# Performance work log

Hardware: AMD Instinct MI355X
Metric: run time of the kernel (lower is better)

The kernel has to match this reference:

```python
import jax, jax.numpy as jnp
import numpy as np

N, E = 20000, 320000
NF, EF = 4, 4
HID, HEADS, MODEL_HID = 128, 4, 128


def _p(key, shape, scale=0.1):
    return scale * jax.random.normal(key, shape, dtype=jnp.float32)


def setup_inputs() -> dict:
    key = jax.random.key(0)
    ks = jax.random.split(key, 32)
    x = jax.random.normal(ks[0], (N, NF), dtype=jnp.float32)
    src = jax.random.randint(ks[1], (E,), 0, N)
    off = jax.random.randint(ks[2], (E,), 1, N)
    dst = (src + off) % N  # no self-loops (PyG removes then re-adds them)
    edge_index = jnp.stack([src, dst]).astype(jnp.int64)
    edge_attr = jax.random.uniform(ks[3], (E, EF), dtype=jnp.float32)
    d = dict(x=x, edge_index=edge_index, edge_attr=edge_attr)
    # input_proj
    d['Wp'] = _p(ks[4], (NF, HID)); d['bp'] = jnp.zeros((HID,), jnp.float32)
    # GAT layer 1: in=HID, heads=HEADS, out=HID, concat
    d['W1'] = _p(ks[5], (HID, HEADS * HID)); d['We1'] = _p(ks[6], (EF, HEADS * HID))
    d['as1'] = _p(ks[7], (HEADS, HID)); d['ad1'] = _p(ks[8], (HEADS, HID)); d['ae1'] = _p(ks[9], (HEADS, HID))
    d['b1'] = jnp.zeros((HEADS * HID,), jnp.float32)
    d['g1'] = jnp.ones((HEADS * HID,), jnp.float32); d['be1'] = jnp.zeros((HEADS * HID,), jnp.float32)
    # GAT layer 2: in=HEADS*HID, heads=1, out=HID, mean
    d['W2'] = _p(ks[10], (HEADS * HID, HID)); d['We2'] = _p(ks[11], (EF, HID))
    d['as2'] = _p(ks[12], (1, HID)); d['ad2'] = _p(ks[13], (1, HID)); d['ae2'] = _p(ks[14], (1, HID))
    d['b2'] = jnp.zeros((HID,), jnp.float32)
    d['g2'] = jnp.ones((HID,), jnp.float32); d['be2'] = jnp.zeros((HID,), jnp.float32)
    # output proj + importance scorer
    d['Wo'] = _p(ks[15], (HID, MODEL_HID)); d['bo'] = jnp.zeros((MODEL_HID,), jnp.float32)
    d['Wi'] = _p(ks[16], (MODEL_HID, 1)); d['bi'] = jnp.zeros((1,), jnp.float32)
    return d


def _layer_norm(x, g, b, eps=1e-5):
    mu = x.mean(-1, keepdims=True)
    v = ((x - mu) ** 2).mean(-1, keepdims=True)
    return (x - mu) * jax.lax.rsqrt(v + eps) * g + b


def _segment_softmax(logits, seg, num):
    m = jax.ops.segment_max(logits, seg, num_segments=num)
    e = jnp.exp(logits - m[seg])
    d = jax.ops.segment_sum(e, seg, num_segments=num)
    return e / d[seg]


def _forward(x, edge_index, edge_attr, Wp, bp, W1, We1, as1, ad1, ae1, b1, g1, be1,
             W2, We2, as2, ad2, ae2, b2, g2, be2, Wo, bo, Wi, bi):
    n = x.shape[0]
    src, dst = edge_index[0], edge_index[1]
    e = edge_attr.shape[0]
    # add_self_loops with fill_value='mean': self-loop attr = mean of incoming edge_attr
    deg = jax.ops.segment_sum(jnp.ones((e,), edge_attr.dtype), dst, num_segments=n)
    loop_attr = jax.ops.segment_sum(edge_attr, dst, num_segments=n) / jnp.maximum(deg, 1.0)[:, None]
    loops = jnp.arange(n)
    src_f = jnp.concatenate([src, loops])
    dst_f = jnp.concatenate([dst, loops])
    ea = jnp.concatenate([edge_attr, loop_attr], axis=0)  # [E+N, EF]

    def gat(h, W, We, a_s, a_d, a_e, bias, heads, out_c, concat):
        xh = (h @ W).reshape(n, heads, out_c)                 # [N,H,C]
        eh = (ea @ We).reshape(-1, heads, out_c)              # [E+N,H,C]
        al_s = (xh * a_s).sum(-1)                             # [N,H]
        al_d = (xh * a_d).sum(-1)                             # [N,H]
        al_e = (eh * a_e).sum(-1)                             # [E+N,H]
        logits = jax.nn.leaky_relu(al_s[src_f] + al_d[dst_f] + al_e, negative_slope=0.2)
        alpha = _segment_softmax(logits, dst_f, n)            # [E+N,H]
        out = jax.ops.segment_sum(xh[src_f] * alpha[..., None], dst_f, num_segments=n)
        out = out.reshape(n, heads * out_c) if concat else out.mean(axis=1)
        return out + bias, alpha

    h = x @ Wp + bp
    h, _ = gat(h, W1, We1, as1, ad1, ae1, b1, HEADS, HID, True)
    h = jax.nn.elu(_layer_norm(h, g1, be1))  # dropout is a no-op in eval
    h, edge_attention = gat(h, W2, We2, as2, ad2, ae2, b2, 1, HID, False)
    h = _layer_norm(h, g2, be2)
    emb = h @ Wo + bo
    importance = jax.nn.sigmoid(emb @ Wi + bi).squeeze(-1)
    return emb, edge_attention, importance


def reference(x, edge_index, edge_attr, Wp, bp, W1, We1, as1, ad1, ae1, b1, g1, be1,
              W2, We2, as2, ad2, ae2, b2, g2, be2, Wo, bo, Wi, bi):
    return _forward(x, edge_index, edge_attr, Wp, bp, W1, We1, as1, ad1, ae1, b1, g1, be1,
                    W2, We2, as2, ad2, ae2, b2, g2, be2, Wo, bo, Wi, bi)
```

## Files before the change

kernel.cpp:

```cpp
#include <hip/hip_runtime.h>
#include <math.h>
#include <stdint.h>

#define N_NODES 20000
#define N_EDGES 320000
#define EN_TOT  340000
#define CAP     160

typedef __attribute__((ext_vector_type(8))) _Float16 half8v;
typedef __attribute__((ext_vector_type(2))) _Float16 half2v;
typedef __attribute__((ext_vector_type(4))) float float4v;

__device__ __forceinline__ ushort f2h(float f) {
    _Float16 h = (_Float16)f;
    return __builtin_bit_cast(ushort, h);
}
__device__ __forceinline__ float h2f(ushort s) {
    return (float)__builtin_bit_cast(_Float16, s);
}

__global__ void k_deg(const int* __restrict__ dst, int* __restrict__ degi) {
    int e = blockIdx.x * 256 + threadIdx.x;
    if (e >= N_EDGES) return;
    atomicAdd(&degi[dst[e]], 1);
}

__global__ __launch_bounds__(1024) void k_scan(const int* __restrict__ degi, int* __restrict__ offsets,
                                               const float* __restrict__ We1, const float* __restrict__ ae1,
                                               const float* __restrict__ We2, const float* __restrict__ ae2,
                                               float* __restrict__ M1, float* __restrict__ m2) {
    __shared__ int s[1024];
    int t = threadIdx.x;
    int n0 = t * 20;
    int tot = 0;
    for (int i = 0; i < 20; i++) {
        int n = n0 + i;
        if (n < N_NODES) tot += degi[n] + 1;
    }
    s[t] = tot;
    __syncthreads();
    for (int off = 1; off < 1024; off <<= 1) {
        int v = (t >= off) ? s[t - off] : 0;
        __syncthreads();
        s[t] += v;
        __syncthreads();
    }
    int run = s[t] - tot;
    for (int i = 0; i < 20; i++) {
        int n = n0 + i;
        if (n < N_NODES) {
            offsets[n] = run;
            run += degi[n] + 1;
        }
    }
    if (t == 1023) offsets[N_NODES] = s[1023];
    if (t < 16) {
        int f = t >> 2, h = t & 3;
        float acc = 0.f;
        for (int c = 0; c < 128; c++) acc += We1[f * 512 + h * 128 + c] * ae1[h * 128 + c];
        M1[f * 4 + h] = acc;
    } else if (t < 20) {
        int f = t - 16;
        float acc = 0.f;
        for (int c = 0; c < 128; c++) acc += We2[f * 128 + c] * ae2[c];
        m2[f] = acc;
    }
}

__global__ void k_fill(const int* __restrict__ src, const int* __restrict__ dst,
                       const int* __restrict__ offsets, int* __restrict__ cursor,
                       int2* __restrict__ csr_se) {
    int i = blockIdx.x * 256 + threadIdx.x;
    if (i >= EN_TOT) return;
    int d, sidx, eid;
    if (i < N_EDGES) { d = dst[i]; sidx = src[i]; eid = i; }
    else { int n = i - N_EDGES; d = n; sidx = n; eid = N_EDGES + n; }
    int pos = offsets[d] + atomicAdd(&cursor[d], 1);
    csr_se[pos] = make_int2(sidx, eid);
}

__global__ __launch_bounds__(256) void k_misc(const int* __restrict__ offsets, const int2* __restrict__ csr_se,
                                              const float* __restrict__ eattr, float* __restrict__ loopattr,
                                              const float* __restrict__ W1, const float* __restrict__ W2,
                                              const float* __restrict__ Wo, ushort* __restrict__ W1T,
                                              ushort* __restrict__ W2T, ushort* __restrict__ WoT,
                                              const float* __restrict__ x, const float* __restrict__ Wp,
                                              const float* __restrict__ bp, ushort* __restrict__ h0h) {
    int b = blockIdx.x;
    int tid = threadIdx.x;
    if (b < 5000) {
        int wv = tid >> 6, l = tid & 63;
        int n = b * 4 + wv;
        if (n >= N_NODES) return;
        int start = offsets[n], end = offsets[n + 1];
        float sx = 0.f, sy = 0.f, sz = 0.f, sw = 0.f;
        for (int p = start + l; p < end; p += 64) {
            int eid = csr_se[p].y;
            if (eid < N_EDGES) {
                float4 e = *(const float4*)&eattr[(size_t)eid * 4];
                sx += e.x; sy += e.y; sz += e.z; sw += e.w;
            }
        }
        for (int off = 32; off; off >>= 1) {
            sx += __shfl_down(sx, off);
            sy += __shfl_down(sy, off);
            sz += __shfl_down(sz, off);
            sw += __shfl_down(sw, off);
        }
        if (l == 0) {
            float inv = 1.0f / fmaxf((float)(end - start - 1), 1.0f);
            float4 o;
            o.x = sx * inv; o.y = sy * inv; o.z = sz * inv; o.w = sw * inv;
            *(float4*)&loopattr[(size_t)n * 4] = o;
        }
    } else if (b < 5576) {
        int i = (b - 5000) * 256 + tid;
        if (i < 512 * 128) {
            int nn = i >> 7, kk = i & 127;
            W1T[i] = f2h(W1[kk * 512 + nn]);
        } else if (i < 2 * 512 * 128) {
            int j = i - 512 * 128;
            int nn = j >> 9, kk = j & 511;
            W2T[j] = f2h(W2[kk * 128 + nn]);
        } else if (i < 2 * 512 * 128 + 128 * 128) {
            int j = i - 2 * 512 * 128;
            int nn = j >> 7, kk = j & 127;
            WoT[j] = f2h(Wo[kk * 128 + nn]);
        }
    } else {
        int n = (b - 5576) * 2 + (tid >> 7);
        int c = tid & 127;
        float acc = bp[c];
#pragma unroll
        for (int f = 0; f < 4; f++) acc += x[n * 4 + f] * Wp[f * 128 + c];
        h0h[(size_t)n * 128 + c] = f2h(acc);
    }
}

__global__ __launch_bounds__(256) void k_gemm_hf(const ushort* __restrict__ A, const ushort* __restrict__ BT,
                                                 float* __restrict__ Cf, ushort* __restrict__ Ch,
                                                 int M, int Nn, int K, const float* __restrict__ bias,
                                                 const float* __restrict__ asv, const float* __restrict__ adv,
                                                 float* __restrict__ outS, float* __restrict__ outD,
                                                 int hstride, const float* __restrict__ sbias) {
    __shared__ ushort As[64 * 64];
    __shared__ ushort Bs[128 * 64];
    __shared__ float redS[4][64];
    __shared__ float redD[4][64];
    const int tid = threadIdx.x;
    const int lane = tid & 63, wid = tid >> 6;
    const int m0 = blockIdx.x * 64, n0 = blockIdx.y * 128;
    float4v acc[4][2];
#pragma unroll
    for (int i = 0; i < 4; i++)
#pragma unroll
        for (int j = 0; j < 2; j++) acc[i][j] = (float4v){0.f, 0.f, 0.f, 0.f};

    for (int k0 = 0; k0 < K; k0 += 64) {
        __syncthreads();
#pragma unroll
        for (int i = 0; i < 2; i++) {
            int c = tid + i * 256;
            int row = c >> 3, sl = c & 7;
            int off = row * 128 + ((sl ^ (row & 7)) << 4);
            uint4 va = make_uint4(0u, 0u, 0u, 0u);
            if (m0 + row < M) va = *(const uint4*)&A[(size_t)(m0 + row) * K + k0 + sl * 8];
            *(uint4*)((char*)As + off) = va;
        }
#pragma unroll
        for (int i = 0; i < 4; i++) {
            int c = tid + i * 256;
            int row = c >> 3, sl = c & 7;
            int off = row * 128 + ((sl ^ (row & 7)) << 4);
            uint4 vb = *(const uint4*)&BT[(size_t)(n0 + row) * K + k0 + sl * 8];
            *(uint4*)((char*)Bs + off) = vb;
        }
        __syncthreads();
#pragma unroll
        for (int kk = 0; kk < 2; kk++) {
            half8v af[4], bq[2];
            int sl = kk * 4 + (lane >> 4);
#pragma unroll
            for (int mi = 0; mi < 4; mi++) {
                int row = (lane & 15) + mi * 16;
                af[mi] = *(const half8v*)((const char*)As + row * 128 + ((sl ^ (row & 7)) << 4));
            }
#pragma unroll
            for (int ni = 0; ni < 2; ni++) {
                int row = wid * 32 + ni * 16 + (lane & 15);
                bq[ni] = *(const half8v*)((const char*)Bs + row * 128 + ((sl ^ (row & 7)) << 4));
            }
#pragma unroll
            for (int mi = 0; mi < 4; mi++)
#pragma unroll
                for (int ni = 0; ni < 2; ni++)
                    acc[mi][ni] = __builtin_amdgcn_mfma_f32_16x16x32_f16(af[mi], bq[ni], acc[mi][ni], 0, 0, 0);
        }
    }
    float bcol[2];
#pragma unroll
    for (int ni = 0; ni < 2; ni++)
        bcol[ni] = bias ? bias[n0 + wid * 32 + ni * 16 + (lane & 15)] : 0.f;
#pragma unroll
    for (int mi = 0; mi < 4; mi++) {
#pragma unroll
        for (int j = 0; j < 4; j++) {
            int row = m0 + mi * 16 + ((lane >> 4) << 2) + j;
            if (row < M) {
#pragma unroll
                for (int ni = 0; ni < 2; ni++) {
                    int col = n0 + wid * 32 + ni * 16 + (lane & 15);
                    float v = acc[mi][ni][j] + bcol[ni];
                    if (Cf) Cf[(size_t)row * Nn + col] = v;
                    if (Ch) Ch[(size_t)row * Nn + col] = f2h(v);
                }
            }
        }
    }
    if (asv) {
        float asl[2], adl[2];
#pragma unroll
        for (int ni = 0; ni < 2; ni++) {
            int col = n0 + wid * 32 + ni * 16 + (lane & 15);
            asl[ni] = asv[col];
            adl[ni] = adv ? adv[col] : 0.f;
        }
        float psv[4][4], pdv[4][4];
#pragma unroll
        for (int mi = 0; mi < 4; mi++)
#pragma unroll
            for (int j = 0; j < 4; j++) {
                float v0 = acc[mi][0][j] + bcol[0];
                float v1 = acc[mi][1][j] + bcol[1];
                psv[mi][j] = v0 * asl[0] + v1 * asl[1];
                pdv[mi][j] = v0 * adl[0] + v1 * adl[1];
            }
#pragma unroll
        for (int off = 1; off < 16; off <<= 1) {
#pragma unroll
            for (int mi = 0; mi < 4; mi++)
#pragma unroll
                for (int j = 0; j < 4; j++) {
                    psv[mi][j] += __shfl_xor(psv[mi][j], off);
                    pdv[mi][j] += __shfl_xor(pdv[mi][j], off);
                }
        }
        if ((lane & 15) == 0) {
#pragma unroll
            for (int mi = 0; mi < 4; mi++)
#pragma unroll
                for (int j = 0; j < 4; j++) {
                    int r = mi * 16 + ((lane >> 4) << 2) + j;
                    redS[wid][r] = psv[mi][j];
                    redD[wid][r] = pdv[mi][j];
                }
        }
        __syncthreads();
        if (tid < 64) {
            int row = m0 + tid;
            if (row < M) {
                float ss = redS[0][tid] + redS[1][tid] + redS[2][tid] + redS[3][tid];
                float dd = redD[0][tid] + redD[1][tid] + redD[2][tid] + redD[3][tid];
                if (sbias) {
                    outS[row] = 1.0f / (1.0f + __expf(-(ss + sbias[0])));
                } else {
                    outS[row * hstride + blockIdx.y] = ss;
                    if (outD) outD[row * hstride + blockIdx.y] = dd;
                }
            }
        }
    }
}

__global__ __launch_bounds__(128) void k_agg1(const int* __restrict__ offsets, const int2* __restrict__ csr_se,
                                              const float* __restrict__ eattr, const float* __restrict__ loopattr,
                                              const float* __restrict__ als, const float* __restrict__ aldv,
                                              const float* __restrict__ M1, const ushort* __restrict__ xhh,
                                              const float* __restrict__ b1, const float* __restrict__ g1,
                                              const float* __restrict__ be1, ushort* __restrict__ h1h) {
    int wv = threadIdx.x >> 6, lane = threadIdx.x & 63;
    int n = blockIdx.x * 2 + wv;
    __shared__ float Lc[2][CAP][4];
    __shared__ int   sSrc[2][CAP];
    __shared__ float mhs[2][4], shs[2][4];

    int start = offsets[n];
    int cnt = offsets[n + 1] - start;

    int hh = lane & 3;
    float aldn = aldv[n * 4 + hh];
    float c0 = M1[hh], c1 = M1[4 + hh], c2 = M1[8 + hh], c3 = M1[12 + hh];
    float m = -1e30f, s = 0.f;
    for (int j = lane >> 2; j < cnt; j += 16) {
        int2 se = csr_se[start + j];
        const float* eap = (se.y < N_EDGES) ? &eattr[(size_t)se.y * 4] : &loopattr[(size_t)(se.y - N_EDGES) * 4];
        float4 e4 = *(const float4*)eap;
        float l = als[se.x * 4 + hh] + aldn + e4.x * c0 + e4.y * c1 + e4.z * c2 + e4.w * c3;
        l = (l >= 0.f) ? l : 0.2f * l;
        Lc[wv][j][hh] = l;
        if (hh == 0) sSrc[wv][j] = se.x;
        float mn = fmaxf(m, l);
        s = s * __expf(m - mn) + __expf(l - mn);
        m = mn;
    }
#pragma unroll
    for (int off = 4; off < 64; off <<= 1) {
        float mo = __shfl_xor(m, off), so = __shfl_xor(s, off);
        float mn = fmaxf(m, mo);
        s = s * __expf(m - mn) + so * __expf(mo - mn);
        m = mn;
    }
    if (lane < 4) { mhs[wv][lane] = m; shs[wv][lane] = 1.0f / s; }

    int tot = cnt * 4;
    for (int idx = lane; idx < tot; idx += 64) {
        int j = idx >> 2, h = idx & 3;
        Lc[wv][j][h] = __expf(Lc[wv][j][h] - mhs[wv][h]) * shs[wv][h];
    }

    half2v hac0 = (half2v)0, hac1 = (half2v)0, hac2 = (half2v)0, hac3 = (half2v)0;
    int hg = lane >> 4;
    uint ch = (uint)lane * 8u;
    int j = 0;
    for (; j + 8 <= cnt; j += 8) {
        _Float16 av[8];
        uint4 vv[8];
#pragma unroll
        for (int t = 0; t < 8; t++) av[t] = (_Float16)Lc[wv][j + t][hg];
#pragma unroll
        for (int t = 0; t < 8; t++) vv[t] = *(const uint4*)&xhh[((uint)sSrc[wv][j + t] << 9) + ch];
#pragma unroll
        for (int t = 0; t < 8; t++) {
            half2v a2 = (half2v){av[t], av[t]};
            const half2v* pv = (const half2v*)&vv[t];
            hac0 = pv[0] * a2 + hac0;
            hac1 = pv[1] * a2 + hac1;
            hac2 = pv[2] * a2 + hac2;
            hac3 = pv[3] * a2 + hac3;
        }
    }
    for (; j < cnt; j++) {
        _Float16 a = (_Float16)Lc[wv][j][hg];
        half2v a2 = (half2v){a, a};
        uint4 v = *(const uint4*)&xhh[((uint)sSrc[wv][j] << 9) + ch];
        const half2v* pv = (const half2v*)&v;
        hac0 = pv[0] * a2 + hac0;
        hac1 = pv[1] * a2 + hac1;
        hac2 = pv[2] * a2 + hac2;
        hac3 = pv[3] * a2 + hac3;
    }

    float4 ba = *(const float4*)&b1[ch];
    float4 bb = *(const float4*)&b1[ch + 4];
    float v0 = (float)hac0[0] + ba.x, v1 = (float)hac0[1] + ba.y;
    float v2 = (float)hac1[0] + ba.z, v3 = (float)hac1[1] + ba.w;
    float v4 = (float)hac2[0] + bb.x, v5 = (float)hac2[1] + bb.y;
    float v6 = (float)hac3[0] + bb.z, v7 = (float)hac3[1] + bb.w;
    float s8 = v0 + v1 + v2 + v3 + v4 + v5 + v6 + v7;
#pragma unroll
    for (int off = 1; off < 64; off <<= 1) s8 += __shfl_xor(s8, off);
    float mu = s8 * (1.0f / 512.0f);
    float d0 = v0 - mu, d1 = v1 - mu, d2 = v2 - mu, d3 = v3 - mu;
    float d4 = v4 - mu, d5 = v5 - mu, d6 = v6 - mu, d7 = v7 - mu;
    float sq = d0 * d0 + d1 * d1 + d2 * d2 + d3 * d3 + d4 * d4 + d5 * d5 + d6 * d6 + d7 * d7;
#pragma unroll
    for (int off = 1; off < 64; off <<= 1) sq += __shfl_xor(sq, off);
    float rstd = rsqrtf(sq * (1.0f / 512.0f) + 1e-5f);
    float4 ga = *(const float4*)&g1[ch];
    float4 gb = *(const float4*)&g1[ch + 4];
    float4 ea = *(const float4*)&be1[ch];
    float4 eb = *(const float4*)&be1[ch + 4];
    float y0 = d0 * rstd * ga.x + ea.x, y1 = d1 * rstd * ga.y + ea.y;
    float y2 = d2 * rstd * ga.z + ea.z, y3 = d3 * rstd * ga.w + ea.w;
    float y4 = d4 * rstd * gb.x + eb.x, y5 = d5 * rstd * gb.y + eb.y;
    float y6 = d6 * rstd * gb.z + eb.z, y7 = d7 * rstd * gb.w + eb.w;
    y0 = (y0 > 0.f) ? y0 : (__expf(y0) - 1.0f);
    y1 = (y1 > 0.f) ? y1 : (__expf(y1) - 1.0f);
    y2 = (y2 > 0.f) ? y2 : (__expf(y2) - 1.0f);
    y3 = (y3 > 0.f) ? y3 : (__expf(y3) - 1.0f);
    y4 = (y4 > 0.f) ? y4 : (__expf(y4) - 1.0f);
    y5 = (y5 > 0.f) ? y5 : (__expf(y5) - 1.0f);
    y6 = (y6 > 0.f) ? y6 : (__expf(y6) - 1.0f);
    y7 = (y7 > 0.f) ? y7 : (__expf(y7) - 1.0f);
    uint4 o;
    o.x = (uint)f2h(y0) | ((uint)f2h(y1) << 16);
    o.y = (uint)f2h(y2) | ((uint)f2h(y3) << 16);
    o.z = (uint)f2h(y4) | ((uint)f2h(y5) << 16);
    o.w = (uint)f2h(y6) | ((uint)f2h(y7) << 16);
    *(uint4*)&h1h[(size_t)n * 512 + ch] = o;
}

__global__ __launch_bounds__(128) void k_agg2(const int* __restrict__ offsets, const int2* __restrict__ csr_se,
                                              const float* __restrict__ eattr, const float* __restrict__ loopattr,
                                              const float* __restrict__ als, const float* __restrict__ aldv,
                                              const float* __restrict__ m2v, const ushort* __restrict__ xh2h,
                                              const float* __restrict__ b2, const float* __restrict__ g2,
                                              const float* __restrict__ be2, float* __restrict__ eaout,
                                              ushort* __restrict__ h2h) {
    int wv = threadIdx.x >> 6, lane = threadIdx.x & 63;
    int n = blockIdx.x * 2 + wv;
    __shared__ float Lc[2][CAP];
    __shared__ int   sS[2][CAP];
    __shared__ int   sE[2][CAP];

    int start = offsets[n];
    int cnt = offsets[n + 1] - start;
    float aldn = aldv[n];
    float c0 = m2v[0], c1 = m2v[1], c2 = m2v[2], c3 = m2v[3];
    float m = -1e30f, s = 0.f;
    for (int j = lane; j < cnt; j += 64) {
        int2 se = csr_se[start + j];
        const float* eap = (se.y < N_EDGES) ? &eattr[(size_t)se.y * 4] : &loopattr[(size_t)(se.y - N_EDGES) * 4];
        float4 e4 = *(const float4*)eap;
        float l = als[se.x] + aldn + e4.x * c0 + e4.y * c1 + e4.z * c2 + e4.w * c3;
        l = (l >= 0.f) ? l : 0.2f * l;
        Lc[wv][j] = l; sS[wv][j] = se.x; sE[wv][j] = se.y;
        float mn = fmaxf(m, l);
        s = s * __expf(m - mn) + __expf(l - mn);
        m = mn;
    }
#pragma unroll
    for (int off = 1; off < 64; off <<= 1) {
        float mo = __shfl_xor(m, off), so = __shfl_xor(s, off);
        float mn = fmaxf(m, mo);
        s = s * __expf(m - mn) + so * __expf(mo - mn);
        m = mn;
    }
    float inv = 1.0f / s;
    for (int j = lane; j < cnt; j += 64) {
        float a = __expf(Lc[wv][j] - m) * inv;
        Lc[wv][j] = a;
        eaout[sE[wv][j]] = a;
    }
    half2v hac = (half2v)0;
    uint ch = (uint)lane * 2u;
    int j = 0;
    for (; j + 8 <= cnt; j += 8) {
        _Float16 av[8];
        uint vv[8];
#pragma unroll
        for (int t = 0; t < 8; t++) av[t] = (_Float16)Lc[wv][j + t];
#pragma unroll
        for (int t = 0; t < 8; t++) vv[t] = *(const uint*)&xh2h[((uint)sS[wv][j + t] << 7) + ch];
#pragma unroll
        for (int t = 0; t < 8; t++) {
            half2v a2 = (half2v){av[t], av[t]};
            half2v pv = __builtin_bit_cast(half2v, vv[t]);
            hac = pv * a2 + hac;
        }
    }
    for (; j < cnt; j++) {
        _Float16 a = (_Float16)Lc[wv][j];
        half2v a2 = (half2v){a, a};
        half2v pv = __builtin_bit_cast(half2v, *(const uint*)&xh2h[((uint)sS[wv][j] << 7) + ch]);
        hac = pv * a2 + hac;
    }
    float2 bb = *(const float2*)&b2[ch];
    float v0 = (float)hac[0] + bb.x, v1 = (float)hac[1] + bb.y;
    float s2 = v0 + v1;
#pragma unroll
    for (int off = 1; off < 64; off <<= 1) s2 += __shfl_xor(s2, off);
    float mu = s2 * (1.0f / 128.0f);
    float d0 = v0 - mu, d1 = v1 - mu;
    float q = d0 * d0 + d1 * d1;
#pragma unroll
    for (int off = 1; off < 64; off <<= 1) q += __shfl_xor(q, off);
    float rstd = rsqrtf(q * (1.0f / 128.0f) + 1e-5f);
    float2 gg = *(const float2*)&g2[ch];
    float2 ee = *(const float2*)&be2[ch];
    float y0 = d0 * rstd * gg.x + ee.x;
    float y1 = d1 * rstd * gg.y + ee.y;
    uint o = (uint)f2h(y0) | ((uint)f2h(y1) << 16);
    *(uint*)&h2h[(size_t)n * 128 + ch] = o;
}

extern "C" void kernel_launch(void* const* d_in, const int* in_sizes, int n_in,
                              void* d_out, int out_size, void* d_ws, size_t ws_size,
                              hipStream_t stream) {
    const float* x    = (const float*)d_in[0];
    const int*   eidx = (const int*)d_in[1];
    const float* eattr= (const float*)d_in[2];
    const float* Wp   = (const float*)d_in[3];
    const float* bp   = (const float*)d_in[4];
    const float* W1   = (const float*)d_in[5];
    const float* We1  = (const float*)d_in[6];
    const float* as1  = (const float*)d_in[7];
    const float* ad1  = (const float*)d_in[8];
    const float* ae1  = (const float*)d_in[9];
    const float* b1   = (const float*)d_in[10];
    const float* g1   = (const float*)d_in[11];
    const float* be1  = (const float*)d_in[12];
    const float* W2   = (const float*)d_in[13];
    const float* We2  = (const float*)d_in[14];
    const float* as2  = (const float*)d_in[15];
    const float* ad2  = (const float*)d_in[16];
    const float* ae2  = (const float*)d_in[17];
    const float* b2   = (const float*)d_in[18];
    const float* g2   = (const float*)d_in[19];
    const float* be2  = (const float*)d_in[20];
    const float* Wo   = (const float*)d_in[21];
    const float* bo   = (const float*)d_in[22];
    const float* Wi   = (const float*)d_in[23];
    const float* bi   = (const float*)d_in[24];

    const int* src = eidx;
    const int* dst = eidx + N_EDGES;

    float* emb_out = (float*)d_out;
    float* ea_out  = emb_out + (size_t)N_NODES * 128;
    float* imp_out = ea_out + EN_TOT;

    char* w = (char*)d_ws;
    auto alloc = [&](size_t bytes) -> void* { void* p = (void*)w; w += (bytes + 255) & ~(size_t)255; return p; };
    ushort* xhh    = (ushort*)alloc((size_t)N_NODES * 512 * 2);
    ushort* h1h    = (ushort*)alloc((size_t)N_NODES * 512 * 2);
    ushort* h0h    = (ushort*)alloc((size_t)N_NODES * 128 * 2);
    ushort* xh2h   = (ushort*)alloc((size_t)N_NODES * 128 * 2);
    ushort* h2h    = (ushort*)alloc((size_t)N_NODES * 128 * 2);
    ushort* W1T    = (ushort*)alloc((size_t)512 * 128 * 2);
    ushort* W2T    = (ushort*)alloc((size_t)128 * 512 * 2);
    ushort* WoT    = (ushort*)alloc((size_t)128 * 128 * 2);
    int2*  csr_se  = (int2*)alloc((size_t)EN_TOT * 8);
    int*   offsets = (int*)alloc((size_t)(N_NODES + 1) * 4);
    int*   cursor  = (int*)alloc((size_t)N_NODES * 4);
    int*   degi    = (int*)alloc((size_t)N_NODES * 4);
    float* loopat  = (float*)alloc((size_t)N_NODES * 4 * 4);
    float* als1v   = (float*)alloc((size_t)N_NODES * 4 * 4);
    float* ald1v   = (float*)alloc((size_t)N_NODES * 4 * 4);
    float* als2v   = (float*)alloc((size_t)N_NODES * 4);
    float* ald2v   = (float*)alloc((size_t)N_NODES * 4);
    float* M1      = (float*)alloc(32 * 4);
    float* m2      = M1 + 16;

    hipMemsetAsync(degi,   0, (size_t)N_NODES * 4, stream);
    hipMemsetAsync(cursor, 0, (size_t)N_NODES * 4, stream);

    k_deg<<<(N_EDGES + 255) / 256, 256, 0, stream>>>(dst, degi);
    k_scan<<<1, 1024, 0, stream>>>(degi, offsets, We1, ae1, We2, ae2, M1, m2);
    k_fill<<<(EN_TOT + 255) / 256, 256, 0, stream>>>(src, dst, offsets, cursor, csr_se);
    k_misc<<<15576, 256, 0, stream>>>(offsets, csr_se, eattr, loopat, W1, W2, Wo,
                                      W1T, W2T, WoT, x, Wp, bp, h0h);

    k_gemm_hf<<<dim3((N_NODES + 63) / 64, 4), 256, 0, stream>>>(h0h, W1T, nullptr, xhh,
                                                                N_NODES, 512, 128, nullptr,
                                                                as1, ad1, als1v, ald1v, 4, nullptr);
    k_agg1<<<N_NODES / 2, 128, 0, stream>>>(offsets, csr_se, eattr, loopat, als1v, ald1v, M1,
                                            xhh, b1, g1, be1, h1h);

    k_gemm_hf<<<dim3((N_NODES + 63) / 64, 1), 256, 0, stream>>>(h1h, W2T, nullptr, xh2h,
                                                                N_NODES, 128, 512, nullptr,
                                                                as2, ad2, als2v, ald2v, 1, nullptr);
    k_agg2<<<N_NODES / 2, 128, 0, stream>>>(offsets, csr_se, eattr, loopat, als2v, ald2v, m2,
                                            xh2h, b2, g2, be2, ea_out, h2h);

    k_gemm_hf<<<dim3((N_NODES + 63) / 64, 1), 256, 0, stream>>>(h2h, WoT, emb_out, nullptr,
                                                                N_NODES, 128, 128, bo,
                                                                Wi, nullptr, imp_out, nullptr, 1, bi);
}
```

Measured before the change: 207.1 us.

## Fuse graph-build kernels into one cooperative kernel and shrink GEMM M-tiles

Replaces the degree, scan, fill and misc kernels with a single cooperative kernel that separates phases with grid-wide syncs. This removes several kernel launches and the cursor memset. Templates the GEMM on BM and uses 32-row tiles for the N=128 GEMMs to get more blocks across CUs. It also clamps per-node edge count to CAP. The scan now runs in a single 256-thread block, and grid.sync adds barrier cost.

```diff
diff --git a/kernel.cpp b/kernel.cpp
--- a/kernel.cpp
+++ b/kernel.cpp
@@ -1,11 +1,15 @@
 #include <hip/hip_runtime.h>
+#include <hip/hip_cooperative_groups.h>
 #include <math.h>
 #include <stdint.h>
+
+namespace cg = cooperative_groups;
 
 #define N_NODES 20000
 #define N_EDGES 320000
 #define EN_TOT  340000
 #define CAP     160
+#define BGRID   1024
 
 typedef __attribute__((ext_vector_type(8))) _Float16 half8v;
 typedef __attribute__((ext_vector_type(2))) _Float16 half2v;
@@ -19,82 +23,110 @@
     return (float)__builtin_bit_cast(_Float16, s);
 }
 
-__global__ void k_deg(const int* __restrict__ dst, int* __restrict__ degi) {
-    int e = blockIdx.x * 256 + threadIdx.x;
-    if (e >= N_EDGES) return;
-    atomicAdd(&degi[dst[e]], 1);
-}
-
-__global__ __launch_bounds__(1024) void k_scan(const int* __restrict__ degi, int* __restrict__ offsets,
-                                               const float* __restrict__ We1, const float* __restrict__ ae1,
-                                               const float* __restrict__ We2, const float* __restrict__ ae2,
-                                               float* __restrict__ M1, float* __restrict__ m2) {
-    __shared__ int s[1024];
-    int t = threadIdx.x;
-    int n0 = t * 20;
-    int tot = 0;
-    for (int i = 0; i < 20; i++) {
-        int n = n0 + i;
-        if (n < N_NODES) tot += degi[n] + 1;
-    }
-    s[t] = tot;
-    __syncthreads();
-    for (int off = 1; off < 1024; off <<= 1) {
-        int v = (t >= off) ? s[t - off] : 0;
+#define ONL(mm, ss, ll) { float _mn = fmaxf(mm, ll); ss = ss * __expf(mm - _mn) + __expf(ll - _mn); mm = _mn; }
+#define MRG(mm, ss, off) { float _mo = __shfl_xor(mm, off), _so = __shfl_xor(ss, off); \
+                           float _mn = fmaxf(mm, _mo); ss = ss * __expf(mm - _mn) + _so * __expf(_mo - _mn); mm = _mn; }
+
+__global__ __launch_bounds__(256, 4) void k_build(const int* __restrict__ src, const int* __restrict__ dst,
+                                                  const float* __restrict__ eattr,
+                                                  int* __restrict__ degi, int* __restrict__ cursor,
+                                                  int* __restrict__ offsets, int2* __restrict__ csr_se,
+                                                  float* __restrict__ loopattr,
+                                                  const float* __restrict__ We1, const float* __restrict__ ae1,
+                                                  const float* __restrict__ We2, const float* __restrict__ ae2,
+                                                  float* __restrict__ M1, float* __restrict__ m2,
+                                                  const float* __restrict__ W1, const float* __restrict__ W2,
+                                                  const float* __restrict__ Wo, ushort* __restrict__ W1T,
+                                                  ushort* __restrict__ W2T, ushort* __restrict__ WoT,
+                                                  const float* __restrict__ x, const float* __restrict__ Wp,
+                                                  const float* __restrict__ bp, ushort* __restrict__ h0h) {
+    cg::grid_group grid = cg::this_grid();
+    __shared__ int sc[256];
+    int b = blockIdx.x, tid = threadIdx.x;
+    int gthreads = BGRID * 256;
+    int gt = b * 256 + tid;
+
+    for (int e2 = gt; e2 < N_EDGES / 2; e2 += gthreads) {
+        int2 d = *(const int2*)&dst[e2 * 2];
+        atomicAdd(&degi[d.x], 1);
+        atomicAdd(&degi[d.y], 1);
+    }
+    for (int n = gt; n < N_NODES; n += gthreads) cursor[n] = 0;
+    grid.sync();
+
+    if (b == 0) {
+        const int PER = (N_NODES + 255) / 256;
+        int n0 = tid * PER;
+        int tot = 0;
+        for (int i = 0; i < PER; i++) {
+            int n = n0 + i;
+            if (n < N_NODES) tot += degi[n] + 1;
+        }
+        sc[tid] = tot;
         __syncthreads();
-        s[t] += v;
-        __syncthreads();
-    }
-    int run = s[t] - tot;
-    for (int i = 0; i < 20; i++) {
-        int n = n0 + i;
-        if (n < N_NODES) {
-            offsets[n] = run;
-            run += degi[n] + 1;
-        }
-    }
-    if (t == 1023) offsets[N_NODES] = s[1023];
-    if (t < 16) {
-        int f = t >> 2, h = t & 3;
-        float acc = 0.f;
-        for (int c = 0; c < 128; c++) acc += We1[f * 512 + h * 128 + c] * ae1[h * 128 + c];
-        M1[f * 4 + h] = acc;
-    } else if (t < 20) {
-        int f = t - 16;
-        float acc = 0.f;
-        for (int c = 0; c < 128; c++) acc += We2[f * 128 + c] * ae2[c];
-        m2[f] = acc;
-    }
-}
-
-__global__ void k_fill(const int* __restrict__ src, const int* __restrict__ dst,
-                       const int* __restrict__ offsets, int* __restrict__ cursor,
-                       int2* __restrict__ csr_se) {
-    int i = blockIdx.x * 256 + threadIdx.x;
-    if (i >= EN_TOT) return;
-    int d, sidx, eid;
-    if (i < N_EDGES) { d = dst[i]; sidx = src[i]; eid = i; }
-    else { int n = i - N_EDGES; d = n; sidx = n; eid = N_EDGES + n; }
-    int pos = offsets[d] + atomicAdd(&cursor[d], 1);
-    csr_se[pos] = make_int2(sidx, eid);
-}
-
-__global__ __launch_bounds__(256) void k_misc(const int* __restrict__ offsets, const int2* __restrict__ csr_se,
-                                              const float* __restrict__ eattr, float* __restrict__ loopattr,
-                                              const float* __restrict__ W1, const float* __restrict__ W2,
-                                              const float* __restrict__ Wo, ushort* __restrict__ W1T,
-                                              ushort* __restrict__ W2T, ushort* __restrict__ WoT,
-                                              const float* __restrict__ x, const float* __restrict__ Wp,
-                                              const float* __restrict__ bp, ushort* __restrict__ h0h) {
-    int b = blockIdx.x;
-    int tid = threadIdx.x;
-    if (b < 5000) {
-        int wv = tid >> 6, l = tid & 63;
-        int n = b * 4 + wv;
-        if (n >= N_NODES) return;
-        int start = offsets[n], end = offsets[n + 1];
+        for (int off = 1; off < 256; off <<= 1) {
+            int v = (tid >= off) ? sc[tid - off] : 0;
+            __syncthreads();
+            sc[tid] += v;
+            __syncthreads();
+        }
+        int run = sc[tid] - tot;
+        for (int i = 0; i < PER; i++) {
+            int n = n0 + i;
+            if (n < N_NODES) { offsets[n] = run; run += degi[n] + 1; }
+        }
+        if (tid == 255) offsets[N_NODES] = sc[255];
+        if (tid < 16) {
+            int f = tid >> 2, h = tid & 3;
+            float acc = 0.f;
+            for (int c = 0; c < 128; c++) acc += We1[f * 512 + h * 128 + c] * ae1[h * 128 + c];
+            M1[f * 4 + h] = acc;
+        } else if (tid < 20) {
+            int f = tid - 16;
+            float acc = 0.f;
+            for (int c = 0; c < 128; c++) acc += We2[f * 128 + c] * ae2[c];
+            m2[f] = acc;
+        }
+    } else {
+        int pstride = (BGRID - 1) * 256;
+        for (int i = (b - 1) * 256 + tid; i < 2 * 512 * 128 + 128 * 128; i += pstride) {
+            if (i < 512 * 128) {
+                int nn = i >> 7, kk = i & 127;
+                W1T[i] = f2h(W1[kk * 512 + nn]);
+            } else if (i < 2 * 512 * 128) {
+                int j = i - 512 * 128;
+                int nn = j >> 9, kk = j & 511;
+                W2T[j] = f2h(W2[kk * 128 + nn]);
+            } else {
+                int j = i - 2 * 512 * 128;
+                int nn = j >> 7, kk = j & 127;
+                WoT[j] = f2h(Wo[kk * 128 + nn]);
+            }
+        }
+        int c = tid & 127;
+        for (int n = (b - 1) * 2 + (tid >> 7); n < N_NODES; n += (BGRID - 1) * 2) {
+            float acc = bp[c];
+#pragma unroll
+            for (int f = 0; f < 4; f++) acc += x[n * 4 + f] * Wp[f * 128 + c];
+            h0h[(size_t)n * 128 + c] = f2h(acc);
+        }
+    }
+    grid.sync();
+
+    for (int i = gt; i < EN_TOT; i += gthreads) {
+        int d, sidx, eid;
+        if (i < N_EDGES) { d = dst[i]; sidx = src[i]; eid = i; }
+        else { int n = i - N_EDGES; d = n; sidx = n; eid = N_EDGES + n; }
+        int pos = offsets[d] + atomicAdd(&cursor[d], 1);
+        csr_se[pos] = make_int2(sidx, eid);
+    }
+    grid.sync();
+
+    int wv = tid >> 6, l = tid & 63;
+    for (int n = b * 4 + wv; n < N_NODES; n += BGRID * 4) {
+        int startp = offsets[n], endp = offsets[n + 1];
         float sx = 0.f, sy = 0.f, sz = 0.f, sw = 0.f;
-        for (int p = start + l; p < end; p += 64) {
+        for (int p = startp + l; p < endp; p += 64) {
             int eid = csr_se[p].y;
             if (eid < N_EDGES) {
                 float4 e = *(const float4*)&eattr[(size_t)eid * 4];
@@ -108,58 +140,39 @@
             sw += __shfl_down(sw, off);
         }
         if (l == 0) {
-            float inv = 1.0f / fmaxf((float)(end - start - 1), 1.0f);
+            float inv = 1.0f / fmaxf((float)(endp - startp - 1), 1.0f);
             float4 o;
             o.x = sx * inv; o.y = sy * inv; o.z = sz * inv; o.w = sw * inv;
             *(float4*)&loopattr[(size_t)n * 4] = o;
         }
-    } else if (b < 5576) {
-        int i = (b - 5000) * 256 + tid;
-        if (i < 512 * 128) {
-            int nn = i >> 7, kk = i & 127;
-            W1T[i] = f2h(W1[kk * 512 + nn]);
-        } else if (i < 2 * 512 * 128) {
-            int j = i - 512 * 128;
-            int nn = j >> 9, kk = j & 511;
-            W2T[j] = f2h(W2[kk * 128 + nn]);
-        } else if (i < 2 * 512 * 128 + 128 * 128) {
-            int j = i - 2 * 512 * 128;
-            int nn = j >> 7, kk = j & 127;
-            WoT[j] = f2h(Wo[kk * 128 + nn]);
-        }
-    } else {
-        int n = (b - 5576) * 2 + (tid >> 7);
-        int c = tid & 127;
-        float acc = bp[c];
-#pragma unroll
-        for (int f = 0; f < 4; f++) acc += x[n * 4 + f] * Wp[f * 128 + c];
-        h0h[(size_t)n * 128 + c] = f2h(acc);
-    }
-}
-
+    }
+}
+
+template<int BM>
 __global__ __launch_bounds__(256) void k_gemm_hf(const ushort* __restrict__ A, const ushort* __restrict__ BT,
                                                  float* __restrict__ Cf, ushort* __restrict__ Ch,
                                                  int M, int Nn, int K, const float* __restrict__ bias,
                                                  const float* __restrict__ asv, const float* __restrict__ adv,
                                                  float* __restrict__ outS, float* __restrict__ outD,
                                                  int hstride, const float* __restrict__ sbias) {
-    __shared__ ushort As[64 * 64];
+    constexpr int MR = BM / 16;
+    __shared__ ushort As[BM * 64];
     __shared__ ushort Bs[128 * 64];
-    __shared__ float redS[4][64];
-    __shared__ float redD[4][64];
+    __shared__ float redS[4][BM];
+    __shared__ float redD[4][BM];
     const int tid = threadIdx.x;
     const int lane = tid & 63, wid = tid >> 6;
-    const int m0 = blockIdx.x * 64, n0 = blockIdx.y * 128;
-    float4v acc[4][2];
-#pragma unroll
-    for (int i = 0; i < 4; i++)
+    const int m0 = blockIdx.x * BM, n0 = blockIdx.y * 128;
+    float4v acc[MR][2];
+#pragma unroll
+    for (int i = 0; i < MR; i++)
 #pragma unroll
         for (int j = 0; j < 2; j++) acc[i][j] = (float4v){0.f, 0.f, 0.f, 0.f};
 
     for (int k0 = 0; k0 < K; k0 += 64) {
         __syncthreads();
 #pragma unroll
-        for (int i = 0; i < 2; i++) {
+        for (int i = 0; i < BM * 8 / 256; i++) {
             int c = tid + i * 256;
             int row = c >> 3, sl = c & 7;
             int off = row * 128 + ((sl ^ (row & 7)) << 4);
@@ -178,10 +191,10 @@
         __syncthreads();
 #pragma unroll
         for (int kk = 0; kk < 2; kk++) {
-            half8v af[4], bq[2];
+            half8v af[MR], bq[2];
             int sl = kk * 4 + (lane >> 4);
 #pragma unroll
-            for (int mi = 0; mi < 4; mi++) {
+            for (int mi = 0; mi < MR; mi++) {
                 int row = (lane & 15) + mi * 16;
                 af[mi] = *(const half8v*)((const char*)As + row * 128 + ((sl ^ (row & 7)) << 4));
             }
@@ -191,7 +204,7 @@
                 bq[ni] = *(const half8v*)((const char*)Bs + row * 128 + ((sl ^ (row & 7)) << 4));
             }
 #pragma unroll
-            for (int mi = 0; mi < 4; mi++)
+            for (int mi = 0; mi < MR; mi++)
 #pragma unroll
                 for (int ni = 0; ni < 2; ni++)
                     acc[mi][ni] = __builtin_amdgcn_mfma_f32_16x16x32_f16(af[mi], bq[ni], acc[mi][ni], 0, 0, 0);
@@ -202,7 +215,7 @@
     for (int ni = 0; ni < 2; ni++)
         bcol[ni] = bias ? bias[n0 + wid * 32 + ni * 16 + (lane & 15)] : 0.f;
 #pragma unroll
-    for (int mi = 0; mi < 4; mi++) {
+    for (int mi = 0; mi < MR; mi++) {
 #pragma unroll
         for (int j = 0; j < 4; j++) {
             int row = m0 + mi * 16 + ((lane >> 4) << 2) + j;
@@ -225,9 +238,9 @@
             asl[ni] = asv[col];
             adl[ni] = adv ? adv[col] : 0.f;
         }
-        float psv[4][4], pdv[4][4];
-#pragma unroll
-        for (int mi = 0; mi < 4; mi++)
+        float psv[MR][4], pdv[MR][4];
+#pragma unroll
+        for (int mi = 0; mi < MR; mi++)
 #pragma unroll
             for (int j = 0; j < 4; j++) {
                 float v0 = acc[mi][0][j] + bcol[0];
@@ -238,7 +251,7 @@
 #pragma unroll
         for (int off = 1; off < 16; off <<= 1) {
 #pragma unroll
-            for (int mi = 0; mi < 4; mi++)
+            for (int mi = 0; mi < MR; mi++)
 #pragma unroll
                 for (int j = 0; j < 4; j++) {
                     psv[mi][j] += __shfl_xor(psv[mi][j], off);
@@ -247,7 +260,7 @@
         }
         if ((lane & 15) == 0) {
 #pragma unroll
-            for (int mi = 0; mi < 4; mi++)
+            for (int mi = 0; mi < MR; mi++)
 #pragma unroll
                 for (int j = 0; j < 4; j++) {
                     int r = mi * 16 + ((lane >> 4) << 2) + j;
@@ -256,7 +269,7 @@
                 }
         }
         __syncthreads();
-        if (tid < 64) {
+        if (tid < BM) {
             int row = m0 + tid;
             if (row < M) {
                 float ss = redS[0][tid] + redS[1][tid] + redS[2][tid] + redS[3][tid];
@@ -285,7 +298,7 @@
     __shared__ float mhs[2][4], shs[2][4];
 
     int start = offsets[n];
-    int cnt = offsets[n + 1] - start;
+    int cnt = min(offsets[n + 1] - start, CAP);
 
     int hh = lane & 3;
     float aldn = aldv[n * 4 + hh];
@@ -299,17 +312,10 @@
         l = (l >= 0.f) ? l : 0.2f * l;
         Lc[wv][j][hh] = l;
         if (hh == 0) sSrc[wv][j] = se.x;
-        float mn = fmaxf(m, l);
-        s = s * __expf(m - mn) + __expf(l - mn);
-        m = mn;
-    }
-#pragma unroll
-    for (int off = 4; off < 64; off <<= 1) {
-        float mo = __shfl_xor(m, off), so = __shfl_xor(s, off);
-        float mn = fmaxf(m, mo);
-        s = s * __expf(m - mn) + so * __expf(mo - mn);
-        m = mn;
-    }
+        ONL(m, s, l);
+    }
+#pragma unroll
+    for (int off = 4; off < 64; off <<= 1) { MRG(m, s, off); }
     if (lane < 4) { mhs[wv][lane] = m; shs[wv][lane] = 1.0f / s; }
 
     int tot = cnt * 4;
@@ -404,7 +410,7 @@
     __shared__ int   sE[2][CAP];
 
     int start = offsets[n];
-    int cnt = offsets[n + 1] - start;
+    int cnt = min(offsets[n + 1] - start, CAP);
     float aldn = aldv[n];
     float c0 = m2v[0], c1 = m2v[1], c2 = m2v[2], c3 = m2v[3];
     float m = -1e30f, s = 0.f;
@@ -415,17 +421,10 @@
         float l = als[se.x] + aldn + e4.x * c0 + e4.y * c1 + e4.z * c2 + e4.w * c3;
         l = (l >= 0.f) ? l : 0.2f * l;
         Lc[wv][j] = l; sS[wv][j] = se.x; sE[wv][j] = se.y;
-        float mn = fmaxf(m, l);
-        s = s * __expf(m - mn) + __expf(l - mn);
-        m = mn;
-    }
-#pragma unroll
-    for (int off = 1; off < 64; off <<= 1) {
-        float mo = __shfl_xor(m, off), so = __shfl_xor(s, off);
-        float mn = fmaxf(m, mo);
-        s = s * __expf(m - mn) + so * __expf(mo - mn);
-        m = mn;
-    }
+        ONL(m, s, l);
+    }
+#pragma unroll
+    for (int off = 1; off < 64; off <<= 1) { MRG(m, s, off); }
     float inv = 1.0f / s;
     for (int j = lane; j < cnt; j += 64) {
         float a = __expf(Lc[wv][j] - m) * inv;
@@ -439,13 +438,13 @@
         _Float16 av[8];
         uint vv[8];
 #pragma unroll
-        for (int t = 0; t < 8; t++) av[t] = (_Float16)Lc[wv][j + t];
-#pragma unroll
-        for (int t = 0; t < 8; t++) vv[t] = *(const uint*)&xh2h[((uint)sS[wv][j + t] << 7) + ch];
-#pragma unroll
-        for (int t = 0; t < 8; t++) {
-            half2v a2 = (half2v){av[t], av[t]};
-            half2v pv = __builtin_bit_cast(half2v, vv[t]);
+        for (int tt = 0; tt < 8; tt++) av[tt] = (_Float16)Lc[wv][j + tt];
+#pragma unroll
+        for (int tt = 0; tt < 8; tt++) vv[tt] = *(const uint*)&xh2h[((uint)sS[wv][j + tt] << 7) + ch];
+#pragma unroll
+        for (int tt = 0; tt < 8; tt++) {
+            half2v a2 = (half2v){av[tt], av[tt]};
+            half2v pv = __builtin_bit_cast(half2v, vv[tt]);
             hac = pv * a2 + hac;
         }
     }
@@ -532,28 +531,32 @@
     float* M1      = (float*)alloc(32 * 4);
     float* m2      = M1 + 16;
 
-    hipMemsetAsync(degi,   0, (size_t)N_NODES * 4, stream);
-    hipMemsetAsync(cursor, 0, (size_t)N_NODES * 4, stream);
-
-    k_deg<<<(N_EDGES + 255) / 256, 256, 0, stream>>>(dst, degi);
-    k_scan<<<1, 1024, 0, stream>>>(degi, offsets, We1, ae1, We2, ae2, M1, m2);
-    k_fill<<<(EN_TOT + 255) / 256, 256, 0, stream>>>(src, dst, offsets, cursor, csr_se);
-    k_misc<<<15576, 256, 0, stream>>>(offsets, csr_se, eattr, loopat, W1, W2, Wo,
-                                      W1T, W2T, WoT, x, Wp, bp, h0h);
-
-    k_gemm_hf<<<dim3((N_NODES + 63) / 64, 4), 256, 0, stream>>>(h0h, W1T, nullptr, xhh,
-                                                                N_NODES, 512, 128, nullptr,
-                                                                as1, ad1, als1v, ald1v, 4, nullptr);
+    hipMemsetAsync(degi, 0, (size_t)N_NODES * 4, stream);
+
+    {
+        void* kargs[] = {
+            (void*)&src, (void*)&dst, (void*)&eattr,
+            (void*)&degi, (void*)&cursor, (void*)&offsets, (void*)&csr_se, (void*)&loopat,
+            (void*)&We1, (void*)&ae1, (void*)&We2, (void*)&ae2, (void*)&M1, (void*)&m2,
+            (void*)&W1, (void*)&W2, (void*)&Wo, (void*)&W1T, (void*)&W2T, (void*)&WoT,
+            (void*)&x, (void*)&Wp, (void*)&bp, (void*)&h0h
+        };
+        hipLaunchCooperativeKernel((const void*)k_build, dim3(BGRID), dim3(256), kargs, 0, stream);
+    }
+
+    k_gemm_hf<64><<<dim3((N_NODES + 63) / 64, 4), 256, 0, stream>>>(h0h, W1T, nullptr, xhh,
+                                                                    N_NODES, 512, 128, nullptr,
+                                                                    as1, ad1, als1v, ald1v, 4, nullptr);
     k_agg1<<<N_NODES / 2, 128, 0, stream>>>(offsets, csr_se, eattr, loopat, als1v, ald1v, M1,
                                             xhh, b1, g1, be1, h1h);
 
-    k_gemm_hf<<<dim3((N_NODES + 63) / 64, 1), 256, 0, stream>>>(h1h, W2T, nullptr, xh2h,
-                                                                N_NODES, 128, 512, nullptr,
-                                                                as2, ad2, als2v, ald2v, 1, nullptr);
+    k_gemm_hf<32><<<dim3((N_NODES + 31) / 32, 1), 256, 0, stream>>>(h1h, W2T, nullptr, xh2h,
+                                                                    N_NODES, 128, 512, nullptr,
+                                                                    as2, ad2, als2v, ald2v, 1, nullptr);
     k_agg2<<<N_NODES / 2, 128, 0, stream>>>(offsets, csr_se, eattr, loopat, als2v, ald2v, m2,
                                             xh2h, b2, g2, be2, ea_out, h2h);
 
-    k_gemm_hf<<<dim3((N_NODES + 63) / 64, 1), 256, 0, stream>>>(h2h, WoT, emb_out, nullptr,
-                                                                N_NODES, 128, 128, bo,
-                                                                Wi, nullptr, imp_out, nullptr, 1, bi);
-}
+    k_gemm_hf<32><<<dim3((N_NODES + 31) / 32, 1), 256, 0, stream>>>(h2h, WoT, emb_out, nullptr,
+                                                                    N_NODES, 128, 128, bo,
+                                                                    Wi, nullptr, imp_out, nullptr, 1, bi);
+}
```

Result: slower. 511.3 us (+146.9%).
